# Performance work log

Hardware: AMD Instinct MI355X
Metric: run time of the kernel (lower is better)

The kernel has to match this reference:

```python
import jax, jax.numpy as jnp
import numpy as np

DIM = 256
B = 8
H = 56
W = 56
K = 2
EPS = 1e-5  # torch BatchNorm2d default eps


def _conv1x1(x, w, b):
    # x: [B,C,H,W], w: [O,C], b: [O]
    return jnp.einsum('oc,bchw->bohw', w, x) + b[None, :, None, None]


def _bn(x, g, be, m, v):
    # inference-mode BatchNorm2d with running stats
    s = g / jnp.sqrt(v + EPS)
    return x * s[None, :, None, None] + (be - m * s)[None, :, None, None]


def _grapher(x, w1, b1, g1, be1, m1, v1, wg, bg, gg, beg, mg, vg, w2, b2, g2, be2, m2, v2):
    # fc1: 1x1 conv + BN
    h = _bn(_conv1x1(x, w1, b1), g1, be1, m1, v1)
    Hh, Ww = h.shape[2], h.shape[3]
    # MRConv4d: running max over circular-shift differences
    # torch.cat([x[:,:,-i:,:], x[:,:,:-i,:]], dim=2) == jnp.roll(x, i, axis=2)
    xj = jnp.zeros_like(h)

    def body_h(c, i):
        return jnp.maximum(c, h - jnp.roll(h, i, axis=2)), None

    xj, _ = jax.lax.scan(body_h, xj, jnp.arange(K, Hh, K))

    def body_w(c, i):
        return jnp.maximum(c, h - jnp.roll(h, i, axis=3)), None

    xj, _ = jax.lax.scan(body_w, xj, jnp.arange(K, Ww, K))

    cat = jnp.concatenate([h, xj], axis=1)  # [B, 2*dim, H, W]
    # MRConv4d.nn: Conv2d(2*dim, 2*dim, 1) -> BN(2*dim) -> GELU (exact erf)
    g = jax.nn.gelu(_bn(_conv1x1(cat, wg, bg), gg, beg, mg, vg), approximate=False)
    # fc2: Conv2d(2*dim, dim, 1) + BN(dim), then residual
    return _bn(_conv1x1(g, w2, b2), g2, be2, m2, v2) + x


def setup_inputs() -> dict:
    key = jax.random.key(0)
    ks = jax.random.split(key, 12)
    d, d2 = DIM, 2 * DIM

    def w(k, o, c):
        return jax.random.normal(k, (o, c), jnp.float32) * np.float32(1.0 / np.sqrt(c))

    return {
        'x': jax.random.normal(ks[0], (B, d, H, W), jnp.float32),
        'w1': w(ks[1], d, d), 'b1': jnp.zeros((d,), jnp.float32),
        'g1': jnp.ones((d,), jnp.float32), 'be1': jnp.zeros((d,), jnp.float32),
        'm1': jax.random.normal(ks[2], (d,), jnp.float32) * 0.1,
        'v1': jax.random.uniform(ks[3], (d,), jnp.float32, 0.5, 1.5),
        'wg': w(ks[4], d2, d2), 'bg': jnp.zeros((d2,), jnp.float32),
        'gg': jnp.ones((d2,), jnp.float32), 'beg': jnp.zeros((d2,), jnp.float32),
        'mg': jax.random.normal(ks[5], (d2,), jnp.float32) * 0.1,
        'vg': jax.random.uniform(ks[6], (d2,), jnp.float32, 0.5, 1.5),
        'w2': w(ks[7], d, d2), 'b2': jnp.zeros((d,), jnp.float32),
        'g2': jnp.ones((d,), jnp.float32), 'be2': jnp.zeros((d,), jnp.float32),
        'm2': jax.random.normal(ks[8], (d,), jnp.float32) * 0.1,
        'v2': jax.random.uniform(ks[9], (d,), jnp.float32, 0.5, 1.5),
    }


def reference(x, w1, b1, g1, be1, m1, v1, wg, bg, gg, beg, mg, vg, w2, b2, g2, be2, m2, v2):
    return _grapher(x, w1, b1, g1, be1, m1, v1, wg, bg, gg, beg, mg, vg, w2, b2, g2, be2, m2, v2)
```

## Files before the change

kernel.cpp:

```cpp
#include <hip/hip_runtime.h>
#include <math.h>

#define SPB 3136
#define NB 8
#define MTOT (NB*SPB)
#define EPS 1e-5f

typedef unsigned short u16;
typedef __attribute__((ext_vector_type(8))) short short8;
typedef __attribute__((ext_vector_type(4))) float float4v;

__device__ __forceinline__ float b2f(u16 v){ unsigned u=((unsigned)v)<<16; float f; __builtin_memcpy(&f,&u,4); return f; }
__device__ __forceinline__ u16 f2b(float f){ unsigned u; __builtin_memcpy(&u,&f,4); u += 0x7fffu + ((u>>16)&1u); return (u16)(u>>16); }
__device__ __forceinline__ float gelu_f(float z){
  float t = 1.5957691216f * z * (1.0f + 0.044715f*z*z);
  return __fdividef(z, 1.0f + __expf(-t));
}

__device__ __forceinline__ void gll16(const u16* g, u16* l){
  __builtin_amdgcn_global_load_lds((const __attribute__((address_space(1))) void*)g,
                                   (__attribute__((address_space(3))) void*)l, 16, 0, 0);
}

__global__ void prep_w_k(const float* __restrict__ w1,const float* __restrict__ wg,const float* __restrict__ w2,
                         const float* b1,const float* g1,const float* be1,const float* m1,const float* v1,
                         const float* bg,const float* gg,const float* beg,const float* mg,const float* vg,
                         const float* b2,const float* g2,const float* be2,const float* m2,const float* v2,
                         u16* __restrict__ w1b,u16* __restrict__ wgb,u16* __restrict__ w2b,float* cst){
  int i = blockIdx.x*256 + threadIdx.x;
  if (i < 65536)  w1b[i] = f2b(w1[i]);
  if (i < 262144) wgb[i] = f2b(wg[i]);
  if (i < 131072) w2b[i] = f2b(w2[i]);
  if (i < 256) {
    float s = g1[i]*rsqrtf(v1[i]+EPS);
    cst[i] = s; cst[256+i] = b1[i]*s + be1[i] - m1[i]*s;
    float s2 = g2[i]*rsqrtf(v2[i]+EPS);
    cst[1536+i] = s2; cst[1792+i] = b2[i]*s2 + be2[i] - m2[i]*s2;
  }
  if (i < 512) {
    float s = gg[i]*rsqrtf(vg[i]+EPS);
    cst[512+i] = s; cst[1024+i] = bg[i]*s + beg[i] - mg[i]*s;
  }
}

__global__ void transpose_x_k(const float* __restrict__ x, u16* __restrict__ xt){
  __shared__ float t[32][33];
  int b = blockIdx.z, ct = blockIdx.y, st = blockIdx.x;
  int ts = threadIdx.x, tc = threadIdx.y;
  #pragma unroll
  for (int i=0;i<4;i++){
    int c = tc + i*8;
    t[c][ts] = x[((size_t)(b*256 + ct*32 + c))*SPB + st*32 + ts];
  }
  __syncthreads();
  #pragma unroll
  for (int i=0;i<4;i++){
    int r = tc + i*8;
    xt[((size_t)(b*SPB + st*32 + r))*256 + ct*32 + ts] = f2b(t[ts][r]);
  }
}

__global__ void minmax_k(const u16* __restrict__ cat, float* __restrict__ rmin, float* __restrict__ cmin){
  int b = blockIdx.x/56, i = blockIdx.x%56, c = threadIdx.x;
  int col = blockIdx.y;
  const u16* base; size_t stride;
  if (!col){ base = cat + ((size_t)(b*SPB + i*56))*512 + c; stride = 512; }
  else     { base = cat + ((size_t)(b*SPB + i))*512 + c;    stride = (size_t)56*512; }
  float a0=3.4e38f,a1=3.4e38f,a2=3.4e38f,a3=3.4e38f;
  for (int j=0;j<56;j+=4){
    a0 = fminf(a0, b2f(base[(size_t)j*stride]));
    a1 = fminf(a1, b2f(base[(size_t)(j+1)*stride]));
    a2 = fminf(a2, b2f(base[(size_t)(j+2)*stride]));
    a3 = fminf(a3, b2f(base[(size_t)(j+3)*stride]));
  }
  float mE = fminf(a0,a2), mO = fminf(a1,a3);
  float* out = col ? cmin : rmin;
  out[((size_t)(b*2+0)*56 + i)*256 + c]=mE;
  out[((size_t)(b*2+1)*56 + i)*256 + c]=mO;
}

__global__ __launch_bounds__(256) void xj_k(u16* __restrict__ cat, const float* __restrict__ rmin, const float* __restrict__ cmin){
  int b = blockIdx.y;
  int t = threadIdx.x;
  int s = blockIdx.x*8 + (t>>5);
  int c0 = (t&31)*8;
  int y = s/56, x = s%56;
  size_t idx = ((size_t)(b*SPB + s))*512;
  short8 h8 = *(const short8*)&cat[idx + c0];
  const float* cp = &cmin[((size_t)(b*2+(y&1))*56 + x)*256 + c0];
  const float* rp = &rmin[((size_t)(b*2+(x&1))*56 + y)*256 + c0];
  float4v cv0 = *(const float4v*)cp, cv1 = *(const float4v*)(cp+4);
  float4v rv0 = *(const float4v*)rp, rv1 = *(const float4v*)(rp+4);
  short8 o;
  #pragma unroll
  for (int j=0;j<8;j++){
    float cm = (j<4) ? cv0[j] : cv1[j-4];
    float rm = (j<4) ? rv0[j] : rv1[j-4];
    o[j] = (short)f2b(fmaxf(0.0f, b2f((u16)h8[j]) - fminf(cm, rm)));
  }
  *(short8*)&cat[idx + 256 + c0] = o;
}

template<int KTOT, int EPI>
__global__ __launch_bounds__(256,2) void gemm_k(
    const u16* __restrict__ Ain, const u16* __restrict__ Wt,
    const float* __restrict__ scale, const float* __restrict__ bias,
    void* __restrict__ outp, const float* __restrict__ resid)
{
  __shared__ __align__(16) u16 smem[36864];
  const int tid = threadIdx.x;
  const int m0 = blockIdx.x * 256;
  const int o0 = blockIdx.y * 128;
  const int lane = tid & 63, wid = tid >> 6;
  const int quad = lane >> 4, l16 = lane & 15;

  float4v acc[4][8];
  #pragma unroll
  for (int i=0;i<4;i++)
    #pragma unroll
    for (int j=0;j<8;j++) acc[i][j] = (float4v){0.f,0.f,0.f,0.f};

  const int row = tid >> 2;
  const int q8s = ((tid & 3) ^ ((tid >> 3) & 3)) * 8;
  const u16* ga0 = Ain + ((size_t)(m0 + row))*KTOT + q8s;
  const u16* gb0 = Wt  + ((size_t)(o0 + row))*KTOT + q8s;
  u16* l8 = smem + tid*8;

  auto STAGE = [&](int kt, int buf){
    u16* b_ = l8 + buf*12288;
    gll16(ga0 + kt,                     b_);
    gll16(ga0 + (size_t) 64*KTOT + kt,  b_ + 2048);
    gll16(ga0 + (size_t)128*KTOT + kt,  b_ + 4096);
    gll16(ga0 + (size_t)192*KTOT + kt,  b_ + 6144);
    gll16(gb0 + kt,                     b_ + 8192);
    gll16(gb0 + (size_t) 64*KTOT + kt,  b_ + 10240);
  };
  const int swz = (l16 >> 1) & 3;
  auto COMPUTE = [&](int buf){
    const u16* A_ = smem + buf*12288;
    const u16* B_ = A_ + 8192;
    const int kq = (quad ^ swz) * 8;
    short8 af[4], bfr[8];
    #pragma unroll
    for (int im=0;im<4;im++) af[im]  = *(const short8*)&A_[(wid*64+im*16+l16)*32 + kq];
    #pragma unroll
    for (int in=0;in<8;in++) bfr[in] = *(const short8*)&B_[(in*16+l16)*32 + kq];
    #pragma unroll
    for (int im=0;im<4;im++)
      #pragma unroll
      for (int in=0;in<8;in++)
        acc[im][in] = __builtin_amdgcn_mfma_f32_16x16x32_bf16(af[im], bfr[in], acc[im][in], 0, 0, 0);
  };

  constexpr int NIT = KTOT / 32;
  STAGE(0, 0);
  STAGE(32, 1);
  #pragma unroll
  for (int t = 0; t < NIT; ++t) {
    __builtin_amdgcn_sched_barrier(0);
    if (t + 1 < NIT) asm volatile("s_waitcnt vmcnt(6) lgkmcnt(0)" ::: "memory");
    else             asm volatile("s_waitcnt vmcnt(0) lgkmcnt(0)" ::: "memory");
    __builtin_amdgcn_s_barrier();
    __builtin_amdgcn_sched_barrier(0);
    if (t + 2 < NIT) STAGE((t+2)*32, (t+2)%3);
    COMPUTE(t%3);
  }
  __syncthreads();

  if (EPI == 1 || EPI == 2) {
    u16* tile = smem;
    #pragma unroll
    for (int im=0;im<4;im++)
      #pragma unroll
      for (int in=0;in<8;in++){
        int ol = in*16 + l16;
        float sc = scale[o0+ol], bi = bias[o0+ol];
        #pragma unroll
        for (int r=0;r<4;r++){
          float v = acc[im][in][r]*sc + bi;
          if (EPI==2) v = gelu_f(v);
          tile[(wid*64+im*16+quad*4+r)*128 + ol] = f2b(v);
        }
      }
    __syncthreads();
    u16* op = (u16*)outp;
    #pragma unroll
    for (int p=0;p<16;p++){
      int chunk = p*256 + tid;
      int rr = chunk >> 4, off = (chunk & 15)*8;
      *(uint4*)&op[((size_t)(m0 + rr))*512 + o0 + off] = *(const uint4*)&tile[rr*128 + off];
    }
  } else {
    float* ftile = (float*)smem;
    float* op = (float*)outp;
    #pragma unroll
    for (int h=0; h<2; h++){
      #pragma unroll
      for (int im=0;im<4;im++)
        #pragma unroll
        for (int in4=0;in4<4;in4++){
          int in = h*4 + in4;
          int c64 = in4*16 + l16;
          int og = o0 + h*64 + c64;
          float sc = scale[og], bi = bias[og];
          float4v v;
          #pragma unroll
          for (int r=0;r<4;r++) v[r] = acc[im][in][r]*sc + bi;
          *(float4v*)&ftile[c64*260 + wid*64 + im*16 + quad*4] = v;
        }
      __syncthreads();
      #pragma unroll
      for (int p=0;p<16;p++){
        int chunk = p*256 + tid;
        int rr = chunk >> 6, off = (chunk & 63)*4;
        int m = m0 + off;
        int b = m / SPB, s = m - b*SPB;
        size_t g = ((size_t)(b*256 + o0 + h*64 + rr))*SPB + s;
        float4v v = *(const float4v*)&ftile[rr*260 + off];
        v.x += resid[g]; v.y += resid[g+1]; v.z += resid[g+2]; v.w += resid[g+3];
        *(float4v*)&op[g] = v;
      }
      __syncthreads();
    }
  }
}

extern "C" void kernel_launch(void* const* d_in, const int* in_sizes, int n_in,
                              void* d_out, int out_size, void* d_ws, size_t ws_size,
                              hipStream_t stream)
{
  const float* x  = (const float*)d_in[0];
  const float* w1 = (const float*)d_in[1];
  const float* b1 = (const float*)d_in[2];
  const float* g1 = (const float*)d_in[3];
  const float* be1= (const float*)d_in[4];
  const float* m1 = (const float*)d_in[5];
  const float* v1 = (const float*)d_in[6];
  const float* wg = (const float*)d_in[7];
  const float* bg = (const float*)d_in[8];
  const float* gg = (const float*)d_in[9];
  const float* beg= (const float*)d_in[10];
  const float* mg = (const float*)d_in[11];
  const float* vg = (const float*)d_in[12];
  const float* w2 = (const float*)d_in[13];
  const float* b2 = (const float*)d_in[14];
  const float* g2 = (const float*)d_in[15];
  const float* be2= (const float*)d_in[16];
  const float* m2 = (const float*)d_in[17];
  const float* v2 = (const float*)d_in[18];

  char* ws = (char*)d_ws;
  size_t off = 0;
  auto alloc = [&](size_t bytes){ void* p = ws + off; off += (bytes + 255) & ~(size_t)255; return p; };
  u16* xt    = (u16*)alloc((size_t)MTOT*256*2);
  u16* catt  = (u16*)alloc((size_t)MTOT*512*2);
  u16* gt    = (u16*)alloc((size_t)MTOT*512*2);
  u16* w1b   = (u16*)alloc((size_t)65536*2);
  u16* wgb   = (u16*)alloc((size_t)262144*2);
  u16* w2b   = (u16*)alloc((size_t)131072*2);
  float* cst = (float*)alloc((size_t)2048*4);
  float* rmin= (float*)alloc((size_t)NB*2*56*256*4);
  float* cmin= (float*)alloc((size_t)NB*2*56*256*4);

  hipLaunchKernelGGL(prep_w_k, dim3(1024), dim3(256), 0, stream,
                     w1,wg,w2, b1,g1,be1,m1,v1, bg,gg,beg,mg,vg, b2,g2,be2,m2,v2,
                     w1b,wgb,w2b, cst);
  hipLaunchKernelGGL(transpose_x_k, dim3(98,8,8), dim3(32,8), 0, stream, x, xt);
  hipLaunchKernelGGL((gemm_k<256,1>), dim3(98,2), dim3(256), 0, stream,
                     xt, w1b, cst+0, cst+256, (void*)catt, (const float*)nullptr);
  hipLaunchKernelGGL(minmax_k, dim3(NB*56,2), dim3(256), 0, stream, catt, rmin, cmin);
  hipLaunchKernelGGL(xj_k, dim3(392, NB), dim3(256), 0, stream, catt, rmin, cmin);
  hipLaunchKernelGGL((gemm_k<512,2>), dim3(98,4), dim3(256), 0, stream,
                     catt, wgb, cst+512, cst+1024, (void*)gt, (const float*)nullptr);
  hipLaunchKernelGGL((gemm_k<512,3>), dim3(98,2), dim3(256), 0, stream,
                     gt, w2b, cst+1536, cst+1792, d_out, x);
}
```

Baseline: 189.5 us.

## Fuse prep kernels, vectorize minmax reduction, add XCD-aware GEMM tile remap

Merges the weight/BN-constant prep kernel with the x transpose kernel into one launch, using extra grid z-slices for the weight conversion. Rewrites minmax so each 32-thread group handles one row/column with 16-byte bf16 vector loads and vector float stores. Remaps GEMM workgroup indices so consecutive tiles sharing the same A rows land on the same XCD for L2 reuse. The minmax grid shrinks to 112 blocks, which may underuse the GPU.

```diff
diff --git a/kernel.cpp b/kernel.cpp
--- a/kernel.cpp
+++ b/kernel.cpp
@@ -22,61 +22,74 @@
                                    (__attribute__((address_space(3))) void*)l, 16, 0, 0);
 }
 
-__global__ void prep_w_k(const float* __restrict__ w1,const float* __restrict__ wg,const float* __restrict__ w2,
-                         const float* b1,const float* g1,const float* be1,const float* m1,const float* v1,
-                         const float* bg,const float* gg,const float* beg,const float* mg,const float* vg,
-                         const float* b2,const float* g2,const float* be2,const float* m2,const float* v2,
-                         u16* __restrict__ w1b,u16* __restrict__ wgb,u16* __restrict__ w2b,float* cst){
-  int i = blockIdx.x*256 + threadIdx.x;
-  if (i < 65536)  w1b[i] = f2b(w1[i]);
-  if (i < 262144) wgb[i] = f2b(wg[i]);
-  if (i < 131072) w2b[i] = f2b(w2[i]);
-  if (i < 256) {
-    float s = g1[i]*rsqrtf(v1[i]+EPS);
-    cst[i] = s; cst[256+i] = b1[i]*s + be1[i] - m1[i]*s;
-    float s2 = g2[i]*rsqrtf(v2[i]+EPS);
-    cst[1536+i] = s2; cst[1792+i] = b2[i]*s2 + be2[i] - m2[i]*s2;
-  }
-  if (i < 512) {
-    float s = gg[i]*rsqrtf(vg[i]+EPS);
-    cst[512+i] = s; cst[1024+i] = bg[i]*s + beg[i] - mg[i]*s;
-  }
-}
-
-__global__ void transpose_x_k(const float* __restrict__ x, u16* __restrict__ xt){
+__global__ void prep_k(const float* __restrict__ x, u16* __restrict__ xt,
+                       const float* __restrict__ w1,const float* __restrict__ wg,const float* __restrict__ w2,
+                       const float* b1,const float* g1,const float* be1,const float* m1,const float* v1,
+                       const float* bg,const float* gg,const float* beg,const float* mg,const float* vg,
+                       const float* b2,const float* g2,const float* be2,const float* m2,const float* v2,
+                       u16* __restrict__ w1b,u16* __restrict__ wgb,u16* __restrict__ w2b,float* cst){
   __shared__ float t[32][33];
-  int b = blockIdx.z, ct = blockIdx.y, st = blockIdx.x;
-  int ts = threadIdx.x, tc = threadIdx.y;
-  #pragma unroll
-  for (int i=0;i<4;i++){
-    int c = tc + i*8;
-    t[c][ts] = x[((size_t)(b*256 + ct*32 + c))*SPB + st*32 + ts];
-  }
-  __syncthreads();
-  #pragma unroll
-  for (int i=0;i<4;i++){
-    int r = tc + i*8;
-    xt[((size_t)(b*SPB + st*32 + r))*256 + ct*32 + ts] = f2b(t[ts][r]);
-  }
-}
-
-__global__ void minmax_k(const u16* __restrict__ cat, float* __restrict__ rmin, float* __restrict__ cmin){
-  int b = blockIdx.x/56, i = blockIdx.x%56, c = threadIdx.x;
+  if (blockIdx.z < 8) {
+    int b = blockIdx.z, ct = blockIdx.y, st = blockIdx.x;
+    int ts = threadIdx.x, tc = threadIdx.y;
+    #pragma unroll
+    for (int i=0;i<4;i++){
+      int c = tc + i*8;
+      t[c][ts] = x[((size_t)(b*256 + ct*32 + c))*SPB + st*32 + ts];
+    }
+    __syncthreads();
+    #pragma unroll
+    for (int i=0;i<4;i++){
+      int r = tc + i*8;
+      xt[((size_t)(b*SPB + st*32 + r))*256 + ct*32 + ts] = f2b(t[ts][r]);
+    }
+  } else {
+    int tid = threadIdx.y*32 + threadIdx.x;
+    int w = ((blockIdx.z-8)*8 + blockIdx.y)*98 + blockIdx.x;
+    int i = w*256 + tid;
+    if (i < 65536)  w1b[i] = f2b(w1[i]);
+    if (i < 262144) wgb[i] = f2b(wg[i]);
+    if (i < 131072) w2b[i] = f2b(w2[i]);
+    if (i < 256) {
+      float s = g1[i]*rsqrtf(v1[i]+EPS);
+      cst[i] = s; cst[256+i] = b1[i]*s + be1[i] - m1[i]*s;
+      float s2 = g2[i]*rsqrtf(v2[i]+EPS);
+      cst[1536+i] = s2; cst[1792+i] = b2[i]*s2 + be2[i] - m2[i]*s2;
+    }
+    if (i < 512) {
+      float s = gg[i]*rsqrtf(vg[i]+EPS);
+      cst[512+i] = s; cst[1024+i] = bg[i]*s + beg[i] - mg[i]*s;
+    }
+  }
+}
+
+__global__ __launch_bounds__(256) void minmax_k(const u16* __restrict__ cat, float* __restrict__ rmin, float* __restrict__ cmin){
+  int id = blockIdx.x*8 + (threadIdx.x>>5);
+  int b = id/56, i = id%56;
+  int c0 = (threadIdx.x&31)*8;
   int col = blockIdx.y;
   const u16* base; size_t stride;
-  if (!col){ base = cat + ((size_t)(b*SPB + i*56))*512 + c; stride = 512; }
-  else     { base = cat + ((size_t)(b*SPB + i))*512 + c;    stride = (size_t)56*512; }
-  float a0=3.4e38f,a1=3.4e38f,a2=3.4e38f,a3=3.4e38f;
-  for (int j=0;j<56;j+=4){
-    a0 = fminf(a0, b2f(base[(size_t)j*stride]));
-    a1 = fminf(a1, b2f(base[(size_t)(j+1)*stride]));
-    a2 = fminf(a2, b2f(base[(size_t)(j+2)*stride]));
-    a3 = fminf(a3, b2f(base[(size_t)(j+3)*stride]));
-  }
-  float mE = fminf(a0,a2), mO = fminf(a1,a3);
+  if (!col){ base = cat + ((size_t)(b*SPB + i*56))*512 + c0; stride = 512; }
+  else     { base = cat + ((size_t)(b*SPB + i))*512 + c0;    stride = (size_t)56*512; }
+  float mE[8], mO[8];
+  #pragma unroll
+  for (int k=0;k<8;k++){ mE[k]=3.4e38f; mO[k]=3.4e38f; }
+  for (int j=0;j<56;j+=2){
+    short8 e = *(const short8*)(base + (size_t)j*stride);
+    short8 o = *(const short8*)(base + (size_t)(j+1)*stride);
+    #pragma unroll
+    for (int k=0;k<8;k++){
+      mE[k] = fminf(mE[k], b2f((u16)e[k]));
+      mO[k] = fminf(mO[k], b2f((u16)o[k]));
+    }
+  }
   float* out = col ? cmin : rmin;
-  out[((size_t)(b*2+0)*56 + i)*256 + c]=mE;
-  out[((size_t)(b*2+1)*56 + i)*256 + c]=mO;
+  float* pE = &out[((size_t)(b*2+0)*56 + i)*256 + c0];
+  float* pO = &out[((size_t)(b*2+1)*56 + i)*256 + c0];
+  *(float4v*)pE     = (float4v){mE[0],mE[1],mE[2],mE[3]};
+  *(float4v*)(pE+4) = (float4v){mE[4],mE[5],mE[6],mE[7]};
+  *(float4v*)pO     = (float4v){mO[0],mO[1],mO[2],mO[3]};
+  *(float4v*)(pO+4) = (float4v){mO[4],mO[5],mO[6],mO[7]};
 }
 
 __global__ __launch_bounds__(256) void xj_k(u16* __restrict__ cat, const float* __restrict__ rmin, const float* __restrict__ cmin){
@@ -101,6 +114,12 @@
   *(short8*)&cat[idx + 256 + c0] = o;
 }
 
+__device__ __forceinline__ int xcd_remap(int orig, int nwg){
+  int q = nwg >> 3, r = nwg & 7, xc = orig & 7, rest = orig >> 3;
+  int base = (xc < r) ? xc*(q+1) : r*(q+1) + (xc-r)*q;
+  return base + rest;
+}
+
 template<int KTOT, int EPI>
 __global__ __launch_bounds__(256,2) void gemm_k(
     const u16* __restrict__ Ain, const u16* __restrict__ Wt,
@@ -109,8 +128,11 @@
 {
   __shared__ __align__(16) u16 smem[36864];
   const int tid = threadIdx.x;
-  const int m0 = blockIdx.x * 256;
-  const int o0 = blockIdx.y * 128;
+  const int nwg = gridDim.x * gridDim.y;
+  const int flat = blockIdx.y * gridDim.x + blockIdx.x;
+  const int s_ = xcd_remap(flat, nwg);
+  const int m0 = (s_ / gridDim.y) * 256;
+  const int o0 = (s_ % gridDim.y) * 128;
   const int lane = tid & 63, wid = tid >> 6;
   const int quad = lane >> 4, l16 = lane & 15;
 
@@ -262,13 +284,12 @@
   float* rmin= (float*)alloc((size_t)NB*2*56*256*4);
   float* cmin= (float*)alloc((size_t)NB*2*56*256*4);
 
-  hipLaunchKernelGGL(prep_w_k, dim3(1024), dim3(256), 0, stream,
-                     w1,wg,w2, b1,g1,be1,m1,v1, bg,gg,beg,mg,vg, b2,g2,be2,m2,v2,
+  hipLaunchKernelGGL(prep_k, dim3(98,8,10), dim3(32,8), 0, stream,
+                     x, xt, w1,wg,w2, b1,g1,be1,m1,v1, bg,gg,beg,mg,vg, b2,g2,be2,m2,v2,
                      w1b,wgb,w2b, cst);
-  hipLaunchKernelGGL(transpose_x_k, dim3(98,8,8), dim3(32,8), 0, stream, x, xt);
   hipLaunchKernelGGL((gemm_k<256,1>), dim3(98,2), dim3(256), 0, stream,
                      xt, w1b, cst+0, cst+256, (void*)catt, (const float*)nullptr);
-  hipLaunchKernelGGL(minmax_k, dim3(NB*56,2), dim3(256), 0, stream, catt, rmin, cmin);
+  hipLaunchKernelGGL(minmax_k, dim3(56,2), dim3(256), 0, stream, catt, rmin, cmin);
   hipLaunchKernelGGL(xj_k, dim3(392, NB), dim3(256), 0, stream, catt, rmin, cmin);
   hipLaunchKernelGGL((gemm_k<512,2>), dim3(98,4), dim3(256), 0, stream,
                      catt, wgb, cst+512, cst+1024, (void*)gt, (const float*)nullptr);
```

Measured after the change: 185.9 us. No clear change (-1.9%).
